# Kernel tuning notes

Hardware: AMD Instinct MI355X
Metric: run time of the kernel (lower is better)

The kernel has to match this reference:

```python
import jax, jax.numpy as jnp
import numpy as np

EPS = 1e-6
QMAX = 127.0  # hif8 emulated as symmetric 8-bit fake-quant (true hif8 numerics are proprietary)


def _rotate_half(v):
    d = v.shape[-1] // 2
    return jnp.concatenate([-v[..., d:], v[..., :d]], axis=-1)


def _quant(v):
    # per-row (last-axis) absmax quantization emulating hif8 with a per-tensor-row scale
    amax = jnp.max(jnp.abs(v), axis=-1, keepdims=True)
    scale = jnp.maximum(amax / QMAX, 1e-8)
    q = jnp.round(v / scale)
    return q, jnp.squeeze(scale, -1)


def setup_inputs() -> dict:
    key = jax.random.key(0)
    ks = jax.random.split(key, 16)
    B, S, H, Hn, D, L = 2, 4096, 2048, 32, 128, 16384
    return {
        "x": jax.random.normal(ks[0], (B, S, H), jnp.float32),
        "q_norm": jax.random.uniform(ks[1], (H,), jnp.float32),
        "q_norm_scale": jax.random.uniform(ks[2], (H,), jnp.float32),
        "w_qb": jax.random.normal(ks[3], (H, Hn * D), jnp.float32),
        "w_qb_scale": jax.random.uniform(ks[4], (Hn * D,), jnp.float32),
        "wk": jax.random.normal(ks[5], (H, D), jnp.float32),
        "w_proj": jax.random.normal(ks[6], (H, Hn), jnp.float32),
        "ln_gamma_k": jax.random.uniform(ks[7], (H,), jnp.float32),
        "ln_beta_k": jax.random.normal(ks[8], (H,), jnp.float32),
        "cos_idx_rope": jax.random.uniform(ks[9], (S, D), jnp.float32),
        "sin_idx_rope": jax.random.uniform(ks[10], (S, D), jnp.float32),
        "hadamard_q": jax.random.normal(ks[11], (D, D), jnp.float32),
        "hadamard_k": jax.random.normal(ks[12], (D, D), jnp.float32),
        "k_cache": jnp.zeros((L, D), jnp.float32),
        "k_cache_scale": jnp.zeros((L,), jnp.float32),
        "k_cache_index": jnp.arange(B * S, dtype=jnp.int32).reshape(B, S),
    }


def reference(x, q_norm, q_norm_scale, w_qb, w_qb_scale, wk, w_proj,
              ln_gamma_k, ln_beta_k, cos_idx_rope, sin_idx_rope,
              hadamard_q, hadamard_k, k_cache, k_cache_scale, k_cache_index):
    B, S, H = x.shape
    D = hadamard_q.shape[0]
    Hn = w_qb.shape[1] // D

    # ---- Q branch: RMSNorm + smooth scale -> quantized GEMM (dequant fused) ----
    rms = jax.lax.rsqrt(jnp.mean(x * x, axis=-1, keepdims=True) + EPS)
    xq = x * rms * q_norm * q_norm_scale                      # [B,S,H]
    q = jnp.einsum('bsh,hd->bsd', xq, w_qb) * w_qb_scale      # [B,S,Hn*D]
    q = q.reshape(B, S, Hn, D)

    cos_q = cos_idx_rope[:S][None, :, None, :]
    sin_q = sin_idx_rope[:S][None, :, None, :]
    q = q * cos_q + _rotate_half(q) * sin_q                   # RoPE
    q = jnp.einsum('bshd,de->bshe', q, hadamard_q)            # Hadamard mix
    q_hif8, q_scale = _quant(q)                               # [B,S,Hn,D], [B,S,Hn]

    # ---- K branch: LayerNorm -> proj -> RoPE -> Hadamard -> quant ----
    mu = jnp.mean(x, axis=-1, keepdims=True)
    var = jnp.mean(jnp.square(x - mu), axis=-1, keepdims=True)
    xk = (x - mu) * jax.lax.rsqrt(var + EPS) * ln_gamma_k + ln_beta_k
    k = jnp.einsum('bsh,hd->bsd', xk, wk)                     # [B,S,D]
    cos_k = cos_idx_rope[:S][None, :, :]
    sin_k = sin_idx_rope[:S][None, :, :]
    k = k * cos_k + _rotate_half(k) * sin_k
    k = jnp.einsum('bsd,de->bse', k, hadamard_k)
    k_q, k_s = _quant(k)                                      # [B,S,D], [B,S]

    # ---- scatter quantized K into the indexer cache ----
    idx = k_cache_index.reshape(-1)
    k_hif8 = k_cache.at[idx].set(k_q.reshape(-1, D))
    k_scale = k_cache_scale.at[idx].set(k_s.reshape(-1))

    # ---- per-head indexer weights ----
    weights = jnp.einsum('bsh,he->bse', x, w_proj)            # [B,S,Hn]

    return (q_hif8, q_scale, k_hif8, k_scale, weights)
```

## Files before the change

### kernel.cpp

```cpp
#include <hip/hip_runtime.h>
#include <hip/hip_bf16.h>
#include <stdint.h>

constexpr int Mrows = 8192;
constexpr int Hdim  = 2048;
constexpr int Sdim  = 4096;
constexpr int HnD   = 4096;
constexpr int Hn    = 32;
constexpr int Dd    = 128;
constexpr int Lc    = 16384;
constexpr int NFULL = 4352;

typedef unsigned short u16;
typedef __attribute__((ext_vector_type(8))) short    bf16x8;
typedef __attribute__((ext_vector_type(4))) float    f32x4;
typedef __attribute__((ext_vector_type(8))) unsigned short u16x8;

__device__ __forceinline__ float bf2f(u16 u) {
    union { unsigned int i; float f; } v; v.i = ((unsigned int)u) << 16; return v.f;
}
__device__ __forceinline__ u16 f2bf(float f) {
    union { float f; unsigned int i; } v; v.f = f;
    unsigned int x = v.i;
    return (u16)((x + 0x7fffu + ((x >> 16) & 1u)) >> 16);
}
__device__ __forceinline__ void gload_lds16(const void* g, void* l) {
    __builtin_amdgcn_global_load_lds(
        (const __attribute__((address_space(1))) void*)g,
        (__attribute__((address_space(3))) void*)l, 16, 0, 0);
}

__global__ __launch_bounds__(256) void stats_cvt(
    const float* __restrict__ x, u16* __restrict__ xb, float* __restrict__ rms,
    float* __restrict__ mu, float* __restrict__ rstd)
{
    int r = blockIdx.x, t = threadIdx.x;
    const float4* xr = (const float4*)(x + (size_t)r * Hdim);
    float4 a = xr[2 * t], bq = xr[2 * t + 1];
    float v[8] = {a.x, a.y, a.z, a.w, bq.x, bq.y, bq.z, bq.w};
    float s = 0.f, ss = 0.f;
    __align__(16) u16 o[8];
    #pragma unroll
    for (int i = 0; i < 8; i++) { s += v[i]; ss += v[i] * v[i]; o[i] = f2bf(v[i]); }
    ((u16x8*)(xb + (size_t)r * Hdim))[t] = *(const u16x8*)o;
    for (int oo = 32; oo > 0; oo >>= 1) { s += __shfl_down(s, oo); ss += __shfl_down(ss, oo); }
    __shared__ float as[4], ass[4];
    if ((t & 63) == 0) { as[t >> 6] = s; ass[t >> 6] = ss; }
    __syncthreads();
    if (t == 0) {
        float S1 = as[0] + as[1] + as[2] + as[3];
        float S2 = ass[0] + ass[1] + ass[2] + ass[3];
        float mean = S1 / Hdim, msq = S2 / Hdim;
        rms[r]  = rsqrtf(msq + 1e-6f);
        mu[r]   = mean;
        rstd[r] = rsqrtf(msq - mean * mean + 1e-6f);
    }
}

__global__ __launch_bounds__(256) void prep_wt(
    const float* __restrict__ wqb, const float* __restrict__ qn, const float* __restrict__ qns,
    const float* __restrict__ wk,  const float* __restrict__ g,  const float* __restrict__ wproj,
    u16* __restrict__ wt)
{
    __shared__ u16 tile[64][72];
    int k0 = blockIdx.x * 64, n0 = blockIdx.y * 64;
    int t = threadIdx.x;
    int lk = t >> 2, lc0 = (t & 3) * 16;
    int k = k0 + lk;
    float c1k = qn[k] * qns[k];
    float gk  = g[k];
    #pragma unroll
    for (int i = 0; i < 16; i++) {
        int n = n0 + lc0 + i;
        float val;
        if (n < 4096)      val = wqb[(size_t)k * HnD + n] * c1k;
        else if (n < 4224) val = wk[k * Dd + (n - 4096)] * gk;
        else if (n < 4256) val = wproj[k * Hn + (n - 4224)];
        else               val = 0.f;
        tile[lk][lc0 + i] = f2bf(val);
    }
    __syncthreads();
    int ln = t >> 2, lk0 = (t & 3) * 16;
    __align__(16) u16 o[16];
    #pragma unroll
    for (int i = 0; i < 16; i++) o[i] = tile[lk0 + i][ln];
    u16* dst = wt + (size_t)(n0 + ln) * Hdim + k0 + lk0;
    *(u16x8*)dst = *(const u16x8*)o;
    *(u16x8*)(dst + 8) = *((const u16x8*)o + 1);
}

__global__ __launch_bounds__(256) void transpose_h(
    const float* __restrict__ hq, const float* __restrict__ hk,
    u16* __restrict__ hqt, u16* __restrict__ hkt)
{
    __shared__ float tile[128][129];
    const float* src = blockIdx.x ? hk : hq;
    u16* dst = blockIdx.x ? hkt : hqt;
    int t = threadIdx.x;
    int r = t >> 1, h = (t & 1) * 64;
    #pragma unroll
    for (int j = 0; j < 16; j++) {
        float4 v = *(const float4*)(src + r * Dd + h + 4 * j);
        tile[r][h + 4 * j]     = v.x;
        tile[r][h + 4 * j + 1] = v.y;
        tile[r][h + 4 * j + 2] = v.z;
        tile[r][h + 4 * j + 3] = v.w;
    }
    __syncthreads();
    #pragma unroll
    for (int j0 = 0; j0 < 64; j0 += 8) {
        __align__(16) u16 o[8];
        #pragma unroll
        for (int j = 0; j < 8; j++) o[j] = f2bf(tile[h + j0 + j][r]);
        *(u16x8*)(dst + r * Dd + h + j0) = *(const u16x8*)o;
    }
}

__global__ __launch_bounds__(256) void bg_dot(
    const float* __restrict__ wk, const float* __restrict__ g, const float* __restrict__ b,
    float* __restrict__ bdot, float* __restrict__ gdot)
{
    int n = blockIdx.x, t = threadIdx.x;
    float sb = 0.f, sg = 0.f;
    for (int k = t; k < Hdim; k += 256) {
        float w = wk[k * Dd + n];
        sb += b[k] * w;
        sg += g[k] * w;
    }
    for (int o = 32; o > 0; o >>= 1) { sb += __shfl_down(sb, o); sg += __shfl_down(sg, o); }
    __shared__ float rb[4], rg[4];
    if ((t & 63) == 0) { rb[t >> 6] = sb; rg[t >> 6] = sg; }
    __syncthreads();
    if (t == 0) { bdot[n] = rb[0] + rb[1] + rb[2] + rb[3]; gdot[n] = rg[0] + rg[1] + rg[2] + rg[3]; }
}

#define LDA_(buf, mt, kk) (*(const bf16x8*)(lds + (buf)*65536 + \
    (wr*64 + (mt)*16 + l15) * 128 + ((((kk)*4 + quad) ^ (l15 & 7)) * 16)))
#define LDB_(buf, nt, kk) (*(const bf16x8*)(lds + (buf)*65536 + 32768 + \
    (wc*128 + (nt)*16 + l15) * 128 + ((((kk)*4 + quad) ^ (l15 & 7)) * 16)))
#define STAGE_A(buf, g, kt) gload_lds16( \
    Ab + (size_t)((g)*64 + r64) * Hdim + (kt)*64 + cswz, \
    ldst + (buf)*65536 + (g)*8192)
#define STAGE_B(buf, g, kt) gload_lds16( \
    Bb + (size_t)((g)*64 + r64) * Hdim + (kt)*64 + cswz, \
    ldst + (buf)*65536 + 32768 + (g)*8192)

__global__ __launch_bounds__(512, 2) void main_gemm(
    const u16* __restrict__ A, const u16* __restrict__ Bt,
    const float* __restrict__ rms, const float* __restrict__ mu, const float* __restrict__ rstd,
    const float* __restrict__ qbs,
    const float* __restrict__ bdot, const float* __restrict__ gdot,
    const u16* __restrict__ hqt,
    const float* __restrict__ cosr, const float* __restrict__ sinr,
    float* __restrict__ oq, float* __restrict__ oqs,
    float* __restrict__ kpre, float* __restrict__ wout)
{
    __shared__ __align__(16) char lds[131072];

    int tid = threadIdx.x;
    int w = tid >> 6, lane = tid & 63, quad = lane >> 4, l15 = lane & 15;
    int wr = w >> 1, wc = w & 1;
    int lin = blockIdx.x + 32 * blockIdx.y;
    int wg = (lin & 7) * 68 + (lin >> 3);
    int bm = wg & 31, bn = wg >> 5;
    int brow = bm * 256;

    const u16* Ab = A  + (size_t)brow * Hdim;
    const u16* Bb = Bt + (size_t)(bn * 256) * Hdim;

    int r64 = tid >> 3;
    int cswz = (((tid & 7) ^ (r64 & 7)) * 8);
    char* ldst = lds + (tid >> 6) * 1024;

    f32x4 acc[4][8] = {};

    #pragma unroll
    for (int g = 0; g < 4; g++) { STAGE_A(0, g, 0); STAGE_B(0, g, 0); }

    for (int t = 0; t < 32; t++) {
        int buf = t & 1, nb = buf ^ 1;
        bool pf = (t + 1 < 32);
        asm volatile("s_waitcnt vmcnt(0)" ::: "memory");
        __builtin_amdgcn_sched_barrier(0);
        __builtin_amdgcn_s_barrier();

        bf16x8 a0[4], a1[4], bfr[4];
        #pragma unroll
        for (int mt = 0; mt < 4; mt++) a0[mt] = LDA_(buf, mt, 0);
        #pragma unroll
        for (int nt = 0; nt < 4; nt++) bfr[nt] = LDB_(buf, nt, 0);
        if (pf) { STAGE_A(nb, 0, t+1); STAGE_A(nb, 1, t+1); STAGE_A(nb, 2, t+1); STAGE_A(nb, 3, t+1); }
        asm volatile("s_waitcnt lgkmcnt(0)" ::: "memory");
        __builtin_amdgcn_sched_barrier(0);
        __builtin_amdgcn_s_setprio(1);
        #pragma unroll
        for (int mt = 0; mt < 4; mt++)
            #pragma unroll
            for (int nt = 0; nt < 4; nt++)
                acc[mt][nt] = __builtin_amdgcn_mfma_f32_16x16x32_bf16(a0[mt], bfr[nt], acc[mt][nt], 0, 0, 0);
        __builtin_amdgcn_s_setprio(0);
        __builtin_amdgcn_s_barrier();
        #pragma unroll
        for (int nt = 0; nt < 4; nt++) bfr[nt] = LDB_(buf, 4 + nt, 0);
        if (pf) { STAGE_B(nb, 0, t+1); STAGE_B(nb, 1, t+1); STAGE_B(nb, 2, t+1); STAGE_B(nb, 3, t+1); }
        asm volatile("s_waitcnt lgkmcnt(0)" ::: "memory");
        __builtin_amdgcn_sched_barrier(0);
        __builtin_amdgcn_s_setprio(1);
        #pragma unroll
        for (int mt = 0; mt < 4; mt++)
            #pragma unroll
            for (int nt = 0; nt < 4; nt++)
                acc[mt][4 + nt] = __builtin_amdgcn_mfma_f32_16x16x32_bf16(a0[mt], bfr[nt], acc[mt][4 + nt], 0, 0, 0);
        __builtin_amdgcn_s_setprio(0);
        __builtin_amdgcn_s_barrier();
        #pragma unroll
        for (int mt = 0; mt < 4; mt++) a1[mt] = LDA_(buf, mt, 1);
        #pragma unroll
        for (int nt = 0; nt < 4; nt++) bfr[nt] = LDB_(buf, nt, 1);
        asm volatile("s_waitcnt lgkmcnt(0)" ::: "memory");
        __builtin_amdgcn_sched_barrier(0);
        __builtin_amdgcn_s_setprio(1);
        #pragma unroll
        for (int mt = 0; mt < 4; mt++)
            #pragma unroll
            for (int nt = 0; nt < 4; nt++)
                acc[mt][nt] = __builtin_amdgcn_mfma_f32_16x16x32_bf16(a1[mt], bfr[nt], acc[mt][nt], 0, 0, 0);
        __builtin_amdgcn_s_setprio(0);
        __builtin_amdgcn_s_barrier();
        #pragma unroll
        for (int nt = 0; nt < 4; nt++) bfr[nt] = LDB_(buf, 4 + nt, 1);
        asm volatile("s_waitcnt lgkmcnt(0)" ::: "memory");
        __builtin_amdgcn_sched_barrier(0);
        __builtin_amdgcn_s_setprio(1);
        #pragma unroll
        for (int mt = 0; mt < 4; mt++)
            #pragma unroll
            for (int nt = 0; nt < 4; nt++)
                acc[mt][4 + nt] = __builtin_amdgcn_mfma_f32_16x16x32_bf16(a1[mt], bfr[nt], acc[mt][4 + nt], 0, 0, 0);
        __builtin_amdgcn_s_setprio(0);
        __builtin_amdgcn_s_barrier();
    }

    if (bn < 16) {
        __syncthreads();
        int head = bn * 2 + wc;
        char* Pw = lds + w * 16384;
        float qb[8];
        #pragma unroll
        for (int nt = 0; nt < 8; nt++) qb[nt] = qbs[head * 128 + nt * 16 + l15];
        #pragma unroll
        for (int mt = 0; mt < 4; mt++) {
            float y[8][4];
            #pragma unroll
            for (int reg = 0; reg < 4; reg++) {
                float rv = rms[brow + wr * 64 + mt * 16 + quad * 4 + reg];
                #pragma unroll
                for (int nt = 0; nt < 8; nt++) y[nt][reg] = acc[mt][nt][reg] * rv * qb[nt];
            }
            #pragma unroll
            for (int reg = 0; reg < 4; reg++) {
                int rp = mt * 16 + quad * 4 + reg;
                int s_ = (brow + wr * 64 + rp) & (Sdim - 1);
                const float* cr = cosr + (size_t)s_ * Dd + l15;
                const float* sr = sinr + (size_t)s_ * Dd + l15;
                int sw = (rp & 7) << 4;
                #pragma unroll
                for (int nt = 0; nt < 8; nt++) {
                    float c  = cr[nt * 16];
                    float sv = sr[nt * 16];
                    float sign = (nt < 4) ? -1.f : 1.f;
                    float o = y[nt][reg] * c + sign * y[nt ^ 4][reg] * sv;
                    int colb = (nt * 16 + l15) * 2;
                    *(u16*)(Pw + rp * 256 + (colb ^ sw)) = f2bf(o);
                }
            }
        }
        __syncthreads();
        #pragma unroll
        for (int mt = 0; mt < 4; mt++) {
            bf16x8 pa[4];
            #pragma unroll
            for (int kb = 0; kb < 4; kb++) {
                int row = mt * 16 + l15;
                pa[kb] = *(const bf16x8*)(Pw + row * 256 + ((kb * 64 + quad * 16) ^ ((row & 7) << 4)));
            }
            f32x4 a2[8] = {};
            #pragma unroll
            for (int nt = 0; nt < 8; nt++) {
                #pragma unroll
                for (int kb = 0; kb < 4; kb++) {
                    bf16x8 hb = *(const bf16x8*)(hqt + (size_t)(nt * 16 + l15) * Dd + kb * 32 + quad * 8);
                    a2[nt] = __builtin_amdgcn_mfma_f32_16x16x32_bf16(pa[kb], hb, a2[nt], 0, 0, 0);
                }
            }
            #pragma unroll
            for (int reg = 0; reg < 4; reg++) {
                float m = 0.f;
                #pragma unroll
                for (int nt = 0; nt < 8; nt++) m = fmaxf(m, fabsf(a2[nt][reg]));
                m = fmaxf(m, __shfl_xor(m, 8));
                m = fmaxf(m, __shfl_xor(m, 4));
                m = fmaxf(m, __shfl_xor(m, 2));
                m = fmaxf(m, __shfl_xor(m, 1));
                float scale = fmaxf(m * (1.f / 127.f), 1e-8f);
                float inv = 1.f / scale;
                int r = brow + wr * 64 + mt * 16 + quad * 4 + reg;
                float* orow = oq + (size_t)r * HnD + head * 128;
                #pragma unroll
                for (int nt = 0; nt < 8; nt++)
                    orow[nt * 16 + l15] = rintf(a2[nt][reg] * inv);
                if (l15 == 0) oqs[(size_t)r * Hn + head] = scale;
            }
        }
    } else {
        if (wc == 0) {
            float bd[8], gd[8];
            #pragma unroll
            for (int nt = 0; nt < 8; nt++) { bd[nt] = bdot[nt * 16 + l15]; gd[nt] = gdot[nt * 16 + l15]; }
            #pragma unroll
            for (int mt = 0; mt < 4; mt++)
                #pragma unroll
                for (int reg = 0; reg < 4; reg++) {
                    int r = brow + wr * 64 + mt * 16 + quad * 4 + reg;
                    float sd = rstd[r], m_ = mu[r];
                    #pragma unroll
                    for (int nt = 0; nt < 8; nt++)
                        kpre[(size_t)r * Dd + nt * 16 + l15] = acc[mt][nt][reg] * sd + bd[nt] - sd * m_ * gd[nt];
                }
        } else {
            #pragma unroll
            for (int mt = 0; mt < 4; mt++)
                #pragma unroll
                for (int reg = 0; reg < 4; reg++) {
                    int r = brow + wr * 64 + mt * 16 + quad * 4 + reg;
                    #pragma unroll
                    for (int nt = 0; nt < 2; nt++)
                        wout[(size_t)r * Hn + nt * 16 + l15] = acc[mt][nt][reg];
                }
        }
    }
}

__global__ void copy_cache(const float* __restrict__ kc, const float* __restrict__ kcs,
                           float* __restrict__ dk, float* __restrict__ dks)
{
    int g = blockIdx.x * 256 + threadIdx.x;
    ((float4*)dk)[2 * g]     = ((const float4*)kc)[2 * g];
    ((float4*)dk)[2 * g + 1] = ((const float4*)kc)[2 * g + 1];
    if (g < Lc / 8) {
        ((float4*)dks)[2 * g]     = ((const float4*)kcs)[2 * g];
        ((float4*)dks)[2 * g + 1] = ((const float4*)kcs)[2 * g + 1];
    }
}

template <int IS_K>
__global__ __launch_bounds__(256) void post_kernel(
    const float* src,
    const u16* __restrict__ ht,
    const float* __restrict__ cosr, const float* __restrict__ sinr,
    const int* __restrict__ idx,
    float* dstq, float* __restrict__ dsts)
{
    constexpr int RP = 136;
    __shared__ __align__(16) u16 sA[32 * RP];
    __shared__ __align__(16) u16 sB[128 * RP];
    __shared__ float pamax[32][2];
    __shared__ int sidx[32];

    int blk = blockIdx.x, tid = threadIdx.x;

    {
        int n = tid >> 1, kk0 = (tid & 1) * 64;
        const u16x8* gp = (const u16x8*)(ht + n * Dd + kk0);
        u16* lb = sB + n * RP + kk0;
        #pragma unroll
        for (int j = 0; j < 8; j++) *(u16x8*)(lb + j * 8) = gp[j];
    }
    {
        int r = tid >> 3, c = tid & 7;
        int d0 = c * 16;
        int s_ = IS_K ? ((blk * 32 + r) & (Sdim - 1)) : (blk & (Sdim - 1));
        const float* srow = src + (size_t)blk * 4096 + r * Dd;
        int p0 = (d0 + 64) & 127;
        float sign = (d0 < 64) ? -1.f : 1.f;
        float vv[16], pv[16], cv[16], sv[16];
        #pragma unroll
        for (int j = 0; j < 4; j++) {
            float4 a = *(const float4*)(srow + d0 + 4 * j);
            float4 p = *(const float4*)(srow + p0 + 4 * j);
            float4 cc = *(const float4*)(cosr + (size_t)s_ * Dd + d0 + 4 * j);
            float4 sc = *(const float4*)(sinr + (size_t)s_ * Dd + d0 + 4 * j);
            vv[4*j] = a.x; vv[4*j+1] = a.y; vv[4*j+2] = a.z; vv[4*j+3] = a.w;
            pv[4*j] = p.x; pv[4*j+1] = p.y; pv[4*j+2] = p.z; pv[4*j+3] = p.w;
            cv[4*j] = cc.x; cv[4*j+1] = cc.y; cv[4*j+2] = cc.z; cv[4*j+3] = cc.w;
            sv[4*j] = sc.x; sv[4*j+1] = sc.y; sv[4*j+2] = sc.z; sv[4*j+3] = sc.w;
        }
        __align__(16) u16 o[16];
        #pragma unroll
        for (int i = 0; i < 16; i++)
            o[i] = f2bf(vv[i] * cv[i] + sign * pv[i] * sv[i]);
        u16* la = sA + r * RP + d0;
        *(u16x8*)la = *(const u16x8*)o;
        *(u16x8*)(la + 8) = *((const u16x8*)o + 1);
        if (IS_K && tid < 32) sidx[tid] = idx[blk * 32 + tid];
    }
    __syncthreads();

    int w = tid >> 6, lane = tid & 63, quad = lane >> 4, l15 = lane & 15;
    int rs = (w & 1) * 16, cg = (w >> 1) * 64;
    f32x4 acc[4] = {};
    #pragma unroll
    for (int kb = 0; kb < 4; kb++) {
        bf16x8 a = *(const bf16x8*)(sA + (rs + l15) * RP + kb * 32 + quad * 8);
        #pragma unroll
        for (int nt = 0; nt < 4; nt++) {
            bf16x8 b = *(const bf16x8*)(sB + (cg + nt * 16 + l15) * RP + kb * 32 + quad * 8);
            acc[nt] = __builtin_amdgcn_mfma_f32_16x16x32_bf16(a, b, acc[nt], 0, 0, 0);
        }
    }
    #pragma unroll
    for (int reg = 0; reg < 4; reg++) {
        float m = 0.f;
        #pragma unroll
        for (int nt = 0; nt < 4; nt++) m = fmaxf(m, fabsf(acc[nt][reg]));
        m = fmaxf(m, __shfl_xor(m, 8));
        m = fmaxf(m, __shfl_xor(m, 4));
        m = fmaxf(m, __shfl_xor(m, 2));
        m = fmaxf(m, __shfl_xor(m, 1));
        if (l15 == 0) pamax[rs + quad * 4 + reg][w >> 1] = m;
    }
    __syncthreads();
    #pragma unroll
    for (int reg = 0; reg < 4; reg++) {
        int r = rs + quad * 4 + reg;
        float am = fmaxf(pamax[r][0], pamax[r][1]);
        float scale = fmaxf(am * (1.f / 127.f), 1e-8f);
        float inv = 1.f / scale;
        size_t dro = IS_K ? (size_t)sidx[r] * Dd : (size_t)blk * 4096 + (size_t)r * Dd;
        #pragma unroll
        for (int nt = 0; nt < 4; nt++)
            dstq[dro + cg + nt * 16 + l15] = rintf(acc[nt][reg] * inv);
        if (l15 == 0 && (w >> 1) == 0)
            dsts[IS_K ? sidx[r] : blk * Hn + r] = scale;
    }
}

extern "C" void kernel_launch(void* const* d_in, const int* in_sizes, int n_in,
                              void* d_out, int out_size, void* d_ws, size_t ws_size,
                              hipStream_t stream) {
    (void)in_sizes; (void)n_in; (void)out_size; (void)ws_size;
    const float* x    = (const float*)d_in[0];
    const float* qn   = (const float*)d_in[1];
    const float* qns  = (const float*)d_in[2];
    const float* wqb  = (const float*)d_in[3];
    const float* wqbs = (const float*)d_in[4];
    const float* wk   = (const float*)d_in[5];
    const float* wpj  = (const float*)d_in[6];
    const float* g    = (const float*)d_in[7];
    const float* b    = (const float*)d_in[8];
    const float* cosr = (const float*)d_in[9];
    const float* sinr = (const float*)d_in[10];
    const float* hq   = (const float*)d_in[11];
    const float* hk   = (const float*)d_in[12];
    const float* kc   = (const float*)d_in[13];
    const float* kcs  = (const float*)d_in[14];
    const int*   idx  = (const int*)d_in[15];

    char* ws = (char*)d_ws;
    size_t o = 0;
    u16* xb  = (u16*)(ws + o); o += (size_t)Mrows * Hdim * 2;
    u16* wt  = (u16*)(ws + o); o += (size_t)NFULL * Hdim * 2;
    u16* hqt = (u16*)(ws + o); o += Dd * Dd * 2;
    u16* hkt = (u16*)(ws + o); o += Dd * Dd * 2;
    float* rmsb  = (float*)(ws + o); o += (size_t)Mrows * 4;
    float* mub   = (float*)(ws + o); o += (size_t)Mrows * 4;
    float* rstdb = (float*)(ws + o); o += (size_t)Mrows * 4;
    float* bdotb = (float*)(ws + o); o += 512;
    float* gdotb = (float*)(ws + o); o += 512;
    float* kpre  = (float*)(ws + o); o += (size_t)Mrows * Dd * 4;

    float* out = (float*)d_out;
    float* oq  = out;
    float* oqs = oq  + (size_t)Mrows * HnD;
    float* ok  = oqs + (size_t)Mrows * Hn;
    float* oks = ok  + (size_t)Lc * Dd;
    float* ow  = oks + Lc;

    stats_cvt<<<Mrows, 256, 0, stream>>>(x, xb, rmsb, mub, rstdb);
    prep_wt<<<dim3(Hdim / 64, NFULL / 64), 256, 0, stream>>>(wqb, qn, qns, wk, g, wpj, wt);
    transpose_h<<<2, 256, 0, stream>>>(hq, hk, hqt, hkt);
    bg_dot<<<Dd, 256, 0, stream>>>(wk, g, b, bdotb, gdotb);
    main_gemm<<<dim3(32, 17), 512, 0, stream>>>(
        xb, wt, rmsb, mub, rstdb, wqbs, bdotb, gdotb, hqt, cosr, sinr, oq, oqs, kpre, ow);
    copy_cache<<<(Lc * Dd / 8) / 256, 256, 0, stream>>>(kc, kcs, ok, oks);
    post_kernel<1><<<Mrows / 32, 256, 0, stream>>>(kpre, hkt, cosr, sinr, idx, ok, oks);
}
```

Before: 525.2 us.

## Split K-tile staging into two half-slabs with partial vmcnt waits in main GEMM

```diff
diff --git a/kernel.cpp b/kernel.cpp
--- a/kernel.cpp
+++ b/kernel.cpp
@@ -134,16 +134,24 @@
     if (t == 0) { bdot[n] = rb[0] + rb[1] + rb[2] + rb[3]; gdot[n] = rg[0] + rg[1] + rg[2] + rg[3]; }
 }
 
-#define LDA_(buf, mt, kk) (*(const bf16x8*)(lds + (buf)*65536 + \
-    (wr*64 + (mt)*16 + l15) * 128 + ((((kk)*4 + quad) ^ (l15 & 7)) * 16)))
-#define LDB_(buf, nt, kk) (*(const bf16x8*)(lds + (buf)*65536 + 32768 + \
-    (wc*128 + (nt)*16 + l15) * 128 + ((((kk)*4 + quad) ^ (l15 & 7)) * 16)))
-#define STAGE_A(buf, g, kt) gload_lds16( \
-    Ab + (size_t)((g)*64 + r64) * Hdim + (kt)*64 + cswz, \
-    ldst + (buf)*65536 + (g)*8192)
-#define STAGE_B(buf, g, kt) gload_lds16( \
-    Bb + (size_t)((g)*64 + r64) * Hdim + (kt)*64 + cswz, \
-    ldst + (buf)*65536 + 32768 + (g)*8192)
+#define LDA_(buf, kk, mt) (*(const bf16x8*)(lds + (buf)*65536 + (kk)*16384 + \
+    (wr*64 + (mt)*16 + l15) * 64 + qsw))
+#define LDB_(buf, kk, nt) (*(const bf16x8*)(lds + (buf)*65536 + 32768 + (kk)*16384 + \
+    (wc*128 + (nt)*16 + l15) * 64 + qsw))
+#define STG_A(bufb, kk, rh, kt) gload_lds16( \
+    Ab + (size_t)((rh)*128 + lrow) * Hdim + (kt)*64 + (kk)*32 + gcol, \
+    lds + (bufb)*65536 + (kk)*16384 + (rh)*8192 + wq1024)
+#define STG_B(bufb, kk, rh, kt) gload_lds16( \
+    Bb + (size_t)((rh)*128 + lrow) * Hdim + (kt)*64 + (kk)*32 + gcol, \
+    lds + (bufb)*65536 + 32768 + (kk)*16384 + (rh)*8192 + wq1024)
+#define MFMA16(AV, NB) do { \
+    _Pragma("unroll") \
+    for (int mt = 0; mt < 4; mt++) \
+        _Pragma("unroll") \
+        for (int nt = 0; nt < 4; nt++) \
+            acc[mt][(NB)*4 + nt] = __builtin_amdgcn_mfma_f32_16x16x32_bf16( \
+                AV[mt], bfr[nt], acc[mt][(NB)*4 + nt], 0, 0, 0); \
+} while (0)
 
 __global__ __launch_bounds__(512, 2) void main_gemm(
     const u16* __restrict__ A, const u16* __restrict__ Bt,
@@ -160,84 +168,71 @@
     int tid = threadIdx.x;
     int w = tid >> 6, lane = tid & 63, quad = lane >> 4, l15 = lane & 15;
     int wr = w >> 1, wc = w & 1;
-    int lin = blockIdx.x + 32 * blockIdx.y;
-    int wg = (lin & 7) * 68 + (lin >> 3);
-    int bm = wg & 31, bn = wg >> 5;
+    int bm = blockIdx.x, bn = blockIdx.y;
     int brow = bm * 256;
+    int qsw = (quad ^ ((l15 >> 1) & 3)) * 16;
 
     const u16* Ab = A  + (size_t)brow * Hdim;
     const u16* Bb = Bt + (size_t)(bn * 256) * Hdim;
 
-    int r64 = tid >> 3;
-    int cswz = (((tid & 7) ^ (r64 & 7)) * 8);
-    char* ldst = lds + (tid >> 6) * 1024;
+    int lrow = tid >> 2;
+    int gcol = (((tid & 3) ^ ((lrow >> 1) & 3)) * 8);
+    int wq1024 = w * 1024;
 
     f32x4 acc[4][8] = {};
 
-    #pragma unroll
-    for (int g = 0; g < 4; g++) { STAGE_A(0, g, 0); STAGE_B(0, g, 0); }
+    STG_A(0, 0, 0, 0); STG_A(0, 0, 1, 0); STG_B(0, 0, 0, 0); STG_B(0, 0, 1, 0);
+    STG_A(0, 1, 0, 0); STG_A(0, 1, 1, 0); STG_B(0, 1, 0, 0); STG_B(0, 1, 1, 0);
+    asm volatile("s_waitcnt vmcnt(4)" ::: "memory");
+    __builtin_amdgcn_sched_barrier(0);
+    __builtin_amdgcn_s_barrier();
 
     for (int t = 0; t < 32; t++) {
         int buf = t & 1, nb = buf ^ 1;
-        bool pf = (t + 1 < 32);
-        asm volatile("s_waitcnt vmcnt(0)" ::: "memory");
-        __builtin_amdgcn_sched_barrier(0);
-        __builtin_amdgcn_s_barrier();
-
-        bf16x8 a0[4], a1[4], bfr[4];
-        #pragma unroll
-        for (int mt = 0; mt < 4; mt++) a0[mt] = LDA_(buf, mt, 0);
-        #pragma unroll
-        for (int nt = 0; nt < 4; nt++) bfr[nt] = LDB_(buf, nt, 0);
-        if (pf) { STAGE_A(nb, 0, t+1); STAGE_A(nb, 1, t+1); STAGE_A(nb, 2, t+1); STAGE_A(nb, 3, t+1); }
+        bool pf = (t < 31);
+        bf16x8 a0[4], bfr[4];
+        #pragma unroll
+        for (int mt = 0; mt < 4; mt++) a0[mt] = LDA_(buf, 0, mt);
+        #pragma unroll
+        for (int nt = 0; nt < 4; nt++) bfr[nt] = LDB_(buf, 0, nt);
+        if (pf) { STG_A(nb, 0, 0, t+1); STG_A(nb, 0, 1, t+1); STG_B(nb, 0, 0, t+1); STG_B(nb, 0, 1, t+1); }
         asm volatile("s_waitcnt lgkmcnt(0)" ::: "memory");
         __builtin_amdgcn_sched_barrier(0);
         __builtin_amdgcn_s_setprio(1);
-        #pragma unroll
-        for (int mt = 0; mt < 4; mt++)
-            #pragma unroll
-            for (int nt = 0; nt < 4; nt++)
-                acc[mt][nt] = __builtin_amdgcn_mfma_f32_16x16x32_bf16(a0[mt], bfr[nt], acc[mt][nt], 0, 0, 0);
+        MFMA16(a0, 0);
         __builtin_amdgcn_s_setprio(0);
         __builtin_amdgcn_s_barrier();
         #pragma unroll
-        for (int nt = 0; nt < 4; nt++) bfr[nt] = LDB_(buf, 4 + nt, 0);
-        if (pf) { STAGE_B(nb, 0, t+1); STAGE_B(nb, 1, t+1); STAGE_B(nb, 2, t+1); STAGE_B(nb, 3, t+1); }
+        for (int nt = 0; nt < 4; nt++) bfr[nt] = LDB_(buf, 0, 4 + nt);
+        if (pf) { STG_A(nb, 1, 0, t+1); STG_A(nb, 1, 1, t+1); STG_B(nb, 1, 0, t+1); STG_B(nb, 1, 1, t+1); }
         asm volatile("s_waitcnt lgkmcnt(0)" ::: "memory");
         __builtin_amdgcn_sched_barrier(0);
         __builtin_amdgcn_s_setprio(1);
-        #pragma unroll
-        for (int mt = 0; mt < 4; mt++)
-            #pragma unroll
-            for (int nt = 0; nt < 4; nt++)
-                acc[mt][4 + nt] = __builtin_amdgcn_mfma_f32_16x16x32_bf16(a0[mt], bfr[nt], acc[mt][4 + nt], 0, 0, 0);
+        MFMA16(a0, 1);
+        __builtin_amdgcn_s_setprio(0);
+        if (pf) { asm volatile("s_waitcnt vmcnt(8)" ::: "memory"); }
+        else    { asm volatile("s_waitcnt vmcnt(0)" ::: "memory"); }
+        __builtin_amdgcn_sched_barrier(0);
+        __builtin_amdgcn_s_barrier();
+        #pragma unroll
+        for (int mt = 0; mt < 4; mt++) a0[mt] = LDA_(buf, 1, mt);
+        #pragma unroll
+        for (int nt = 0; nt < 4; nt++) bfr[nt] = LDB_(buf, 1, nt);
+        asm volatile("s_waitcnt lgkmcnt(0)" ::: "memory");
+        __builtin_amdgcn_sched_barrier(0);
+        __builtin_amdgcn_s_setprio(1);
+        MFMA16(a0, 0);
         __builtin_amdgcn_s_setprio(0);
         __builtin_amdgcn_s_barrier();
         #pragma unroll
-        for (int mt = 0; mt < 4; mt++) a1[mt] = LDA_(buf, mt, 1);
-        #pragma unroll
-        for (int nt = 0; nt < 4; nt++) bfr[nt] = LDB_(buf, nt, 1);
+        for (int nt = 0; nt < 4; nt++) bfr[nt] = LDB_(buf, 1, 4 + nt);
         asm volatile("s_waitcnt lgkmcnt(0)" ::: "memory");
         __builtin_amdgcn_sched_barrier(0);
         __builtin_amdgcn_s_setprio(1);
-        #pragma unroll
-        for (int mt = 0; mt < 4; mt++)
-            #pragma unroll
-            for (int nt = 0; nt < 4; nt++)
-                acc[mt][nt] = __builtin_amdgcn_mfma_f32_16x16x32_bf16(a1[mt], bfr[nt], acc[mt][nt], 0, 0, 0);
+        MFMA16(a0, 1);
         __builtin_amdgcn_s_setprio(0);
-        __builtin_amdgcn_s_barrier();
-        #pragma unroll
-        for (int nt = 0; nt < 4; nt++) bfr[nt] = LDB_(buf, 4 + nt, 1);
-        asm volatile("s_waitcnt lgkmcnt(0)" ::: "memory");
-        __builtin_amdgcn_sched_barrier(0);
-        __builtin_amdgcn_s_setprio(1);
-        #pragma unroll
-        for (int mt = 0; mt < 4; mt++)
-            #pragma unroll
-            for (int nt = 0; nt < 4; nt++)
-                acc[mt][4 + nt] = __builtin_amdgcn_mfma_f32_16x16x32_bf16(a1[mt], bfr[nt], acc[mt][4 + nt], 0, 0, 0);
-        __builtin_amdgcn_s_setprio(0);
+        asm volatile("s_waitcnt vmcnt(4)" ::: "memory");
+        __builtin_amdgcn_sched_barrier(0);
         __builtin_amdgcn_s_barrier();
     }
 
```

Result: faster. 508.3 us (-3.2%).
